# Kernel tuning notes

Hardware: AMD Instinct MI355X
Metric: run time of the kernel (lower is better)

The kernel has to match this reference:

```python
import jax, jax.numpy as jnp
import numpy as np

D_MODEL = 2048
N_HEADS = 8
HEAD_DIM = D_MODEL // N_HEADS
SCALING = HEAD_DIM ** -0.5


def setup_inputs() -> dict:
    key = jax.random.key(0)
    ks = jax.random.split(key, 9)
    B, S, D = 2, 2048, D_MODEL
    std = D ** -0.5
    inp = {"x": jax.random.normal(ks[0], (B, S, D), dtype=jnp.float32)}
    names = ["Wq", "Wk", "Wv", "Wo"]
    for i, n in enumerate(names):
        inp[n] = jax.random.normal(ks[1 + i], (D, D), dtype=jnp.float32) * std
        inp["b" + n[1]] = jax.random.normal(ks[5 + i], (D,), dtype=jnp.float32) * 0.01
    return inp


def reference(x, Wq, bq, Wk, bk, Wv, bv, Wo, bo):
    B, S, D = x.shape
    H, hd = N_HEADS, HEAD_DIM

    def proj(W, b):
        # nn.Linear: x @ W.T + b, then split heads -> [B, H, S, hd]
        y = jnp.einsum("bsd,ed->bse", x, W) + b
        return y.reshape(B, S, H, hd).transpose(0, 2, 1, 3)

    q = proj(Wq, bq)
    k = proj(Wk, bk)
    v = proj(Wv, bv)

    # scaled QK^T: [B, H, S, S]
    attn_weights = jnp.einsum("bhqd,bhkd->bhqk", q, k) * SCALING
    causal = jnp.tril(jnp.ones((S, S), dtype=bool))  # [S, S]
    attn_weights = jnp.where(causal[None, None], attn_weights, -jnp.inf)
    attn_probs = jax.nn.softmax(attn_weights, axis=-1)

    out = jnp.einsum("bhqk,bhkd->bhqd", attn_probs, v)  # [B, H, S, hd]
    out = out.transpose(0, 2, 1, 3).reshape(B, S, D)
    out = jnp.einsum("bsd,ed->bse", out, Wo) + bo
    return (out, attn_probs)
```

## Files before the change

### kernel.cpp

```cpp
#include <hip/hip_runtime.h>
#include <cstdint>
#include <cstddef>

typedef _Float16 f16;
typedef __attribute__((ext_vector_type(4))) _Float16 f16x4;
typedef __attribute__((ext_vector_type(8))) _Float16 f16x8;
typedef __attribute__((ext_vector_type(4))) float f32x4;

#define NB 2
#define SEQ 2048
#define DM 2048
#define NH 8
#define HD 256
#define MT (NB * SEQ)

#define QSCALE 0.09016844f
#define CEXP   23.08312065f

__device__ __forceinline__ void gload16(const f16* g, f16* l) {
    __builtin_amdgcn_global_load_lds(
        (const __attribute__((address_space(1))) uint32_t*)(const void*)g,
        (__attribute__((address_space(3))) uint32_t*)(void*)l,
        16, 0, 0);
}

__global__ __launch_bounds__(256) void k_cvt5(
    const float* __restrict__ x, const float* __restrict__ Wq,
    const float* __restrict__ Wk, const float* __restrict__ Wv,
    const float* __restrict__ Wo,
    f16* __restrict__ xh, f16* __restrict__ Wqh, f16* __restrict__ Wkh,
    f16* __restrict__ Wvh, f16* __restrict__ Woh) {
    const int total = (MT * DM + 4 * DM * DM) / 4;
    for (int q = blockIdx.x * blockDim.x + threadIdx.x; q < total;
         q += gridDim.x * blockDim.x) {
        int i = q * 4;
        const float* src; f16* dst; int off;
        if (i < MT * DM) { src = x; dst = xh; off = i; }
        else {
            int j = i - MT * DM;
            int w = j >> 22;
            off = j & ((1 << 22) - 1);
            src = (w == 0) ? Wq : (w == 1) ? Wk : (w == 2) ? Wv : Wo;
            dst = (w == 0) ? Wqh : (w == 1) ? Wkh : (w == 2) ? Wvh : Woh;
        }
        f32x4 v = *(const f32x4*)(src + off);
        f16x4 h;
        h[0] = (f16)v[0]; h[1] = (f16)v[1]; h[2] = (f16)v[2]; h[3] = (f16)v[3];
        *(f16x4*)(dst + off) = h;
    }
}

__device__ __forceinline__ void stage3(const f16* __restrict__ A,
                                       const f16* __restrict__ B,
                                       int m0, int n0, int k0,
                                       f16* AL, f16* BL, int tid, int half) {
#pragma unroll
    for (int jj = 0; jj < 2; ++jj) {
        int j = half * 2 + jj;
        int flat = j * 4096 + tid * 8;
        int r = flat >> 6, c = flat & 63;
        int cs = c ^ ((r & 7) << 3);
        gload16(A + (size_t)(m0 + r) * DM + k0 + cs,
                AL + j * 4096 + (tid >> 6) * 512);
    }
    {
        int j = half;
        int flat = j * 4096 + tid * 8;
        int r = flat >> 6, c = flat & 63;
        int cs = c ^ ((r & 7) << 3);
        gload16(B + (size_t)(n0 + r) * DM + k0 + cs,
                BL + j * 4096 + (tid >> 6) * 512);
    }
}

__device__ __forceinline__ f16x8 rdfrag(const f16* buf, int rowbase, int lr,
                                        int lg, int kk) {
    int row = rowbase + lr;
    int c = (kk * 32 + lg * 8) ^ ((lr & 7) << 3);
    return *(const f16x8*)&buf[row * 64 + c];
}

__device__ __forceinline__ void gemm256x128_core(const f16* __restrict__ A,
                                                 const f16* __restrict__ B,
                                                 int m0, int n0,
                                                 f16* AL, f16* BL,
                                                 f32x4 acc[4][4]) {
    const int tid = threadIdx.x, wave = tid >> 6, lane = tid & 63;
    const int wm = wave >> 1, wn = wave & 1;
    const int lr = lane & 15, lg = lane >> 4;
    const int nt = DM / 64;

    stage3(A, B, m0, n0, 0, AL, BL, tid, 0);
    stage3(A, B, m0, n0, 0, AL, BL, tid, 1);
    stage3(A, B, m0, n0, 64, AL + 16384, BL + 8192, tid, 0);
    stage3(A, B, m0, n0, 64, AL + 16384, BL + 8192, tid, 1);
    asm volatile("s_waitcnt vmcnt(6)" ::: "memory");
    __builtin_amdgcn_s_barrier();
    __builtin_amdgcn_sched_barrier(0);

    for (int kt = 0; kt < nt; ++kt) {
        const f16* Ab = AL + (kt % 3) * 16384;
        const f16* Bb = BL + (kt % 3) * 8192;
        const int arb = wm * 64, brb = wn * 64;

#pragma unroll
        for (int ph = 0; ph < 2; ++ph) {
            f16x8 af[4], bf[4];
#pragma unroll
            for (int mf = 0; mf < 4; ++mf)
                af[mf] = rdfrag(Ab, arb + mf * 16, lr, lg, ph);
#pragma unroll
            for (int nf = 0; nf < 4; ++nf)
                bf[nf] = rdfrag(Bb, brb + nf * 16, lr, lg, ph);

            if (kt + 2 < nt)
                stage3(A, B, m0, n0, (kt + 2) * 64,
                       AL + ((kt + 2) % 3) * 16384,
                       BL + ((kt + 2) % 3) * 8192, tid, ph);

            __builtin_amdgcn_sched_barrier(0);
            if (ph == 1) {
                if (kt + 2 < nt)
                    asm volatile("s_waitcnt vmcnt(6)" ::: "memory");
                else if (kt + 1 < nt)
                    asm volatile("s_waitcnt vmcnt(0)" ::: "memory");
            }
            __builtin_amdgcn_s_barrier();
            asm volatile("s_waitcnt lgkmcnt(0)" ::: "memory");
            __builtin_amdgcn_sched_barrier(0);

            __builtin_amdgcn_s_setprio(1);
#pragma unroll
            for (int mi = 0; mi < 4; ++mi)
#pragma unroll
                for (int nj = 0; nj < 4; ++nj)
                    acc[mi][nj] = __builtin_amdgcn_mfma_f32_16x16x32_f16(
                        af[mi], bf[nj], acc[mi][nj], 0, 0, 0);
            __builtin_amdgcn_s_setprio(0);
            __builtin_amdgcn_s_barrier();
        }
    }
}

__global__ __launch_bounds__(512, 1) void k_proj_qkv(
    const f16* __restrict__ xh, const f16* __restrict__ Wq,
    const f16* __restrict__ Wk, const f16* __restrict__ Wv,
    const float* __restrict__ bq, const float* __restrict__ bk,
    const float* __restrict__ bv,
    f16* __restrict__ Qh, f16* __restrict__ Kh, f16* __restrict__ Vth) {
    __shared__ __align__(16) f16 AL[3 * 16384];
    __shared__ __align__(16) f16 BL[3 * 8192];
    const int mode = blockIdx.z;
    const f16* W = (mode == 0) ? Wq : (mode == 1) ? Wk : Wv;
    const float* bias = (mode == 0) ? bq : (mode == 1) ? bk : bv;

    const int phys = blockIdx.x + 16 * blockIdx.y;
    const int xcdq = phys & 7, idx = phys >> 3;
    const int m0 = (xcdq * 2 + (idx >> 4)) * 256;
    const int n0 = (idx & 15) * 128;

    f32x4 acc[4][4];
#pragma unroll
    for (int mi = 0; mi < 4; ++mi)
#pragma unroll
        for (int nj = 0; nj < 4; ++nj) acc[mi][nj] = (f32x4){0.f, 0.f, 0.f, 0.f};

    gemm256x128_core(xh, W, m0, n0, AL, BL, acc);

    const int lane = threadIdx.x & 63, wave = threadIdx.x >> 6;
    const int wm = wave >> 1, wn = wave & 1;
    const int lr = lane & 15, lg = lane >> 4;
#pragma unroll
    for (int nj = 0; nj < 4; ++nj) {
        int n = n0 + wn * 64 + nj * 16 + lr;
        float bb = bias[n];
        int h = n >> 8, d = n & 255;
#pragma unroll
        for (int mi = 0; mi < 4; ++mi) {
#pragma unroll
            for (int i = 0; i < 4; ++i) {
                int m = m0 + wm * 64 + mi * 16 + lg * 4 + i;
                int b = m >> 11, s = m & 2047;
                float v = acc[mi][nj][i] + bb;
                size_t bh = (size_t)(b * NH + h);
                if (mode == 0)
                    Qh[((bh * SEQ + s) << 8) + d] = (f16)(v * QSCALE);
                else if (mode == 1)
                    Kh[((bh * SEQ + s) << 8) + d] = (f16)v;
                else
                    Vth[((bh * HD + d) << 11) + s] = (f16)v;
            }
        }
    }
}

__global__ __launch_bounds__(512, 1) void k_proj_o(
    const f16* __restrict__ Oh, const f16* __restrict__ Wo,
    const float* __restrict__ bo, float* __restrict__ out) {
    __shared__ __align__(16) f16 AL[3 * 16384];
    __shared__ __align__(16) f16 BL[3 * 8192];

    const int phys = blockIdx.x + 16 * blockIdx.y;
    const int xcdq = phys & 7, idx = phys >> 3;
    const int m0 = (xcdq * 2 + (idx >> 4)) * 256;
    const int n0 = (idx & 15) * 128;

    f32x4 acc[4][4];
#pragma unroll
    for (int mi = 0; mi < 4; ++mi)
#pragma unroll
        for (int nj = 0; nj < 4; ++nj) acc[mi][nj] = (f32x4){0.f, 0.f, 0.f, 0.f};

    gemm256x128_core(Oh, Wo, m0, n0, AL, BL, acc);

    const int lane = threadIdx.x & 63, wave = threadIdx.x >> 6;
    const int wm = wave >> 1, wn = wave & 1;
    const int lr = lane & 15, lg = lane >> 4;
#pragma unroll
    for (int nj = 0; nj < 4; ++nj) {
        int n = n0 + wn * 64 + nj * 16 + lr;
        float bb = bo[n];
#pragma unroll
        for (int mi = 0; mi < 4; ++mi) {
#pragma unroll
            for (int i = 0; i < 4; ++i) {
                int m = m0 + wm * 64 + mi * 16 + lg * 4 + i;
                out[(size_t)m * DM + n] = acc[mi][nj][i] + bb;
            }
        }
    }
}

__device__ __forceinline__ void stageK(const f16* __restrict__ Kb, int kt,
                                       f16* buf, int wave, int lane) {
#pragma unroll
    for (int j = 0; j < 8; ++j) {
        int base = (j * 4 + wave) << 9;
        int flat = base + (lane << 3);
        int r = flat >> 8;
        int c = (flat & 255) ^ ((r & 7) << 3);
        gload16(Kb + (size_t)(kt * 64 + r) * HD + c, buf + base);
    }
}
__device__ __forceinline__ void stageV(const f16* __restrict__ Vb, int kt,
                                       f16* buf, int wave, int lane) {
#pragma unroll
    for (int j = 0; j < 8; ++j) {
        int base = (j * 4 + wave) << 9;
        int flat = base + (lane << 3);
        int rv = flat >> 6;
        int cv = (flat & 63) ^ ((rv & 3) << 3);
        gload16(Vb + ((size_t)rv << 11) + kt * 64 + cv, buf + base);
    }
}

__global__ __launch_bounds__(256, 2) void k_attn(
    const f16* __restrict__ Qh, const f16* __restrict__ Kh,
    const f16* __restrict__ Vth, float* __restrict__ P,
    f16* __restrict__ Oh) {
    __shared__ __align__(16) f16 B0[64 * 256];
    __shared__ __align__(16) f16 B1[64 * 256];
    __shared__ __align__(16) f16 Ps[4][16][72];

    const int bid = blockIdx.x;
    const int xcd = bid & 7;
    const int slot = bid >> 3;
    const int psel = slot >> 5;
    const int s5 = slot & 31;
    const int qb = psel ? s5 : (31 - s5);
    const int bhid = xcd * 2 + psel;
    const int b = bhid >> 3, h = bhid & 7;

    const int q0 = qb * 64;
    const int tid = threadIdx.x, wave = tid >> 6, lane = tid & 63;
    const int lr = lane & 15, lg = lane >> 4;
    const size_t bh = (size_t)bhid;
    const f16* Qb = Qh + (bh << 19);
    const f16* Kb = Kh + (bh << 19);
    const f16* Vb = Vth + (bh << 19);
    float* Pb = P + (bh << 22);

    const int kswz = (lr & 7) << 3;
    const int vswz = (lr & 3) << 3;

    f16x8 aq[8];
    {
        const f16* qrow = Qb + (size_t)(q0 + wave * 16 + lr) * HD + lg * 8;
#pragma unroll
        for (int kk = 0; kk < 8; ++kk) aq[kk] = *(const f16x8*)(qrow + kk * 32);
    }

    const int rowb = q0 + wave * 16 + lg * 4;
    const int nt = qb + 1;

    float psum[4] = {0.f, 0.f, 0.f, 0.f};

    stageK(Kb, 0, B0, wave, lane);
    for (int kt = 0; kt < nt; ++kt) {
        f16* cur = (kt & 1) ? B1 : B0;
        f16* nxt = (kt & 1) ? B0 : B1;
        if (kt + 1 < nt) {
            stageK(Kb, kt + 1, nxt, wave, lane);
            asm volatile("s_waitcnt vmcnt(8)" ::: "memory");
        } else {
            asm volatile("s_waitcnt vmcnt(0)" ::: "memory");
        }
        __builtin_amdgcn_s_barrier();
        __builtin_amdgcn_sched_barrier(0);

        f32x4 s[4];
#pragma unroll
        for (int nj = 0; nj < 4; ++nj) s[nj] = (f32x4){0.f, 0.f, 0.f, 0.f};
        __builtin_amdgcn_s_setprio(1);
#pragma unroll
        for (int kk = 0; kk < 8; ++kk) {
#pragma unroll
            for (int nj = 0; nj < 4; ++nj) {
                f16x8 bk = *(const f16x8*)&cur[(nj * 16 + lr) * 256 +
                                               ((kk * 32 + lg * 8) ^ kswz)];
                s[nj] = __builtin_amdgcn_mfma_f32_16x16x32_f16(aq[kk], bk, s[nj], 0, 0, 0);
            }
        }
        __builtin_amdgcn_s_setprio(0);
        if (kt < qb) {
#pragma unroll
            for (int i = 0; i < 4; ++i)
#pragma unroll
                for (int nj = 0; nj < 4; ++nj)
                    psum[i] += exp2f(s[nj][i] - CEXP);
        } else {
            const int colb = kt * 64 + lr;
#pragma unroll
            for (int i = 0; i < 4; ++i) {
                int row = rowb + i;
#pragma unroll
                for (int nj = 0; nj < 4; ++nj)
                    psum[i] += (colb + nj * 16 <= row) ? exp2f(s[nj][i] - CEXP) : 0.f;
            }
        }
        asm volatile("" ::: "memory");
        __builtin_amdgcn_s_barrier();
        __builtin_amdgcn_sched_barrier(0);
    }

    float inv[4];
#pragma unroll
    for (int i = 0; i < 4; ++i) {
        float l = psum[i];
        l += __shfl_xor(l, 1);
        l += __shfl_xor(l, 2);
        l += __shfl_xor(l, 4);
        l += __shfl_xor(l, 8);
        inv[i] = 1.f / l;
    }

    f32x4 o[16];
#pragma unroll
    for (int n = 0; n < 16; ++n) o[n] = (f32x4){0.f, 0.f, 0.f, 0.f};

    stageK(Kb, 0, B0, wave, lane);
    for (int kt = 0; kt < nt; ++kt) {
        stageV(Vb, kt, B1, wave, lane);
        if (kt == 0) asm volatile("s_waitcnt vmcnt(8)" ::: "memory");
        else         asm volatile("s_waitcnt vmcnt(10)" ::: "memory");
        __builtin_amdgcn_s_barrier();
        __builtin_amdgcn_sched_barrier(0);

        f32x4 s[4];
#pragma unroll
        for (int nj = 0; nj < 4; ++nj) s[nj] = (f32x4){0.f, 0.f, 0.f, 0.f};
        __builtin_amdgcn_s_setprio(1);
#pragma unroll
        for (int kk = 0; kk < 8; ++kk) {
#pragma unroll
            for (int nj = 0; nj < 4; ++nj) {
                f16x8 bk = *(const f16x8*)&B0[(nj * 16 + lr) * 256 +
                                              ((kk * 32 + lg * 8) ^ kswz)];
                s[nj] = __builtin_amdgcn_mfma_f32_16x16x32_f16(aq[kk], bk, s[nj], 0, 0, 0);
            }
        }
        __builtin_amdgcn_s_setprio(0);
        if (kt < qb) {
#pragma unroll
            for (int i = 0; i < 4; ++i)
#pragma unroll
                for (int nj = 0; nj < 4; ++nj) {
                    float pv = exp2f(s[nj][i] - CEXP) * inv[i];
                    Ps[wave][lg * 4 + i][nj * 16 + lr] = (f16)pv;
                }
        } else {
#pragma unroll
            for (int i = 0; i < 4; ++i) {
                int row = rowb + i;
#pragma unroll
                for (int nj = 0; nj < 4; ++nj) {
                    int col = kt * 64 + nj * 16 + lr;
                    float pv = (col <= row) ? exp2f(s[nj][i] - CEXP) * inv[i] : 0.f;
                    Ps[wave][lg * 4 + i][nj * 16 + lr] = (f16)pv;
                }
            }
        }
        asm volatile("s_waitcnt vmcnt(0)" ::: "memory");
        __builtin_amdgcn_s_barrier();
        __builtin_amdgcn_sched_barrier(0);

        if (kt + 1 < nt) stageK(Kb, kt + 1, B0, wave, lane);

        __builtin_amdgcn_s_setprio(1);
#pragma unroll
        for (int kk2 = 0; kk2 < 2; ++kk2) {
            f16x8 pa = *(const f16x8*)&Ps[wave][lr][kk2 * 32 + lg * 8];
#pragma unroll
            for (int n = 0; n < 16; ++n) {
                f16x8 bv = *(const f16x8*)&B1[(n * 16 + lr) * 64 +
                                              ((kk2 * 32 + lg * 8) ^ vswz)];
                o[n] = __builtin_amdgcn_mfma_f32_16x16x32_f16(pa, bv, o[n], 0, 0, 0);
            }
        }
        __builtin_amdgcn_s_setprio(0);

#pragma unroll
        for (int h2 = 0; h2 < 2; ++h2) {
            int rr = h2 * 8 + (lane >> 3);
            int cc = (lane & 7) * 8;
            f16x8 ph = *(const f16x8*)&Ps[wave][rr][cc];
            int row = q0 + wave * 16 + rr;
            float* dst = Pb + (size_t)row * SEQ + kt * 64 + cc;
            f32x4 lo = {(float)ph[0], (float)ph[1], (float)ph[2], (float)ph[3]};
            f32x4 hi = {(float)ph[4], (float)ph[5], (float)ph[6], (float)ph[7]};
            *(f32x4*)dst = lo;
            *(f32x4*)(dst + 4) = hi;
        }

        asm volatile("" ::: "memory");
        __builtin_amdgcn_s_barrier();
        __builtin_amdgcn_sched_barrier(0);
    }

    int kstart = (qb + 1) * 64;
    if (kstart < SEQ) {
        f32x4 z = (f32x4){0.f, 0.f, 0.f, 0.f};
        for (int r = 0; r < 64; ++r) {
            float* rp = Pb + (size_t)(q0 + r) * SEQ;
            for (int c = kstart + tid * 4; c < SEQ; c += 1024)
                *(f32x4*)(rp + c) = z;
        }
    }

#pragma unroll
    for (int n = 0; n < 16; ++n) {
#pragma unroll
        for (int i = 0; i < 4; ++i) {
            int row = rowb + i;
            int d = n * 16 + lr;
            Oh[((size_t)b * SEQ + row) * DM + h * HD + d] = (f16)o[n][i];
        }
    }
}

extern "C" void kernel_launch(void* const* d_in, const int* in_sizes, int n_in,
                              void* d_out, int out_size, void* d_ws, size_t ws_size,
                              hipStream_t stream) {
    const float* x  = (const float*)d_in[0];
    const float* Wq = (const float*)d_in[1];
    const float* bq = (const float*)d_in[2];
    const float* Wk = (const float*)d_in[3];
    const float* bk = (const float*)d_in[4];
    const float* Wv = (const float*)d_in[5];
    const float* bv = (const float*)d_in[6];
    const float* Wo = (const float*)d_in[7];
    const float* bo = (const float*)d_in[8];

    float* out  = (float*)d_out;
    float* Pout = out + (size_t)MT * DM;

    f16* xh  = (f16*)Pout;
    f16* Wqh = xh + (size_t)MT * DM;
    f16* Wkh = Wqh + (size_t)DM * DM;
    f16* Wvh = Wkh + (size_t)DM * DM;

    f16* ws16 = (f16*)d_ws;
    f16* Woh = ws16;
    f16* Qh  = Woh + (size_t)DM * DM;
    f16* Kh  = Qh + (size_t)8388608;
    f16* Vth = Kh + (size_t)8388608;
    f16* Oh  = Vth + (size_t)8388608;
    if (ws_size < (size_t)(4194304 + 4 * 8388608) * sizeof(f16)) return;

    k_cvt5<<<2048, 256, 0, stream>>>(x, Wq, Wk, Wv, Wo, xh, Wqh, Wkh, Wvh, Woh);

    dim3 g1(DM / 128, MT / 256, 3);
    k_proj_qkv<<<g1, 512, 0, stream>>>(xh, Wqh, Wkh, Wvh, bq, bk, bv, Qh, Kh, Vth);

    k_attn<<<dim3(512), 256, 0, stream>>>(Qh, Kh, Vth, Pout, Oh);

    dim3 g3(DM / 128, MT / 256, 1);
    k_proj_o<<<g3, 512, 0, stream>>>(Oh, Woh, bo, out);
}
```

Baseline: 349.4 us.

## Split softmax row-sum pass into separate kernel parallelized over key chunks

The first pass of the attention kernel, which computes softmax denominators with a fixed-max exp, moves into a new k_rowsum kernel. That kernel splits each query block's key tiles across 4 chunks in a second grid dimension and writes per-chunk partial sums to workspace. The attention kernel then reads and adds the four partials instead of recomputing QK^T for the denominator. This raises parallelism for the causal-imbalanced first pass, but it adds a kernel launch, drops the double-buffered K staging in that pass, and reloads Q and K in a separate kernel.

```diff
diff --git a/kernel.cpp b/kernel.cpp
--- a/kernel.cpp
+++ b/kernel.cpp
@@ -254,10 +254,97 @@
     }
 }
 
+__global__ __launch_bounds__(256, 4) void k_rowsum(
+    const f16* __restrict__ Qh, const f16* __restrict__ Kh,
+    float* __restrict__ partial) {
+    __shared__ __align__(16) f16 Kl[64 * 256];
+
+    const int bid = blockIdx.x;
+    const int xcd = bid & 7;
+    const int slot = bid >> 3;
+    const int psel = slot >> 5;
+    const int s5 = slot & 31;
+    const int qb = psel ? s5 : (31 - s5);
+    const int bhid = xcd * 2 + psel;
+    const int chunk = blockIdx.y;
+
+    const int q0 = qb * 64;
+    const int tid = threadIdx.x, wave = tid >> 6, lane = tid & 63;
+    const int lr = lane & 15, lg = lane >> 4;
+    const size_t bh = (size_t)bhid;
+    const f16* Qb = Qh + (bh << 19);
+    const f16* Kb = Kh + (bh << 19);
+
+    const int kswz = (lr & 7) << 3;
+
+    f16x8 aq[8];
+    {
+        const f16* qrow = Qb + (size_t)(q0 + wave * 16 + lr) * HD + lg * 8;
+#pragma unroll
+        for (int kk = 0; kk < 8; ++kk) aq[kk] = *(const f16x8*)(qrow + kk * 32);
+    }
+    const int rowb = q0 + wave * 16 + lg * 4;
+    const int nt = qb + 1;
+
+    float psum[4] = {0.f, 0.f, 0.f, 0.f};
+
+    for (int t = chunk; t < nt; t += 4) {
+        stageK(Kb, t, Kl, wave, lane);
+        asm volatile("s_waitcnt vmcnt(0)" ::: "memory");
+        __builtin_amdgcn_s_barrier();
+        __builtin_amdgcn_sched_barrier(0);
+
+        f32x4 s[4];
+#pragma unroll
+        for (int nj = 0; nj < 4; ++nj) s[nj] = (f32x4){0.f, 0.f, 0.f, 0.f};
+        __builtin_amdgcn_s_setprio(1);
+#pragma unroll
+        for (int kk = 0; kk < 8; ++kk) {
+#pragma unroll
+            for (int nj = 0; nj < 4; ++nj) {
+                f16x8 bk = *(const f16x8*)&Kl[(nj * 16 + lr) * 256 +
+                                              ((kk * 32 + lg * 8) ^ kswz)];
+                s[nj] = __builtin_amdgcn_mfma_f32_16x16x32_f16(aq[kk], bk, s[nj], 0, 0, 0);
+            }
+        }
+        __builtin_amdgcn_s_setprio(0);
+        if (t < qb) {
+#pragma unroll
+            for (int i = 0; i < 4; ++i)
+#pragma unroll
+                for (int nj = 0; nj < 4; ++nj)
+                    psum[i] += exp2f(s[nj][i] - CEXP);
+        } else {
+            const int colb = t * 64 + lr;
+#pragma unroll
+            for (int i = 0; i < 4; ++i) {
+                int row = rowb + i;
+#pragma unroll
+                for (int nj = 0; nj < 4; ++nj)
+                    psum[i] += (colb + nj * 16 <= row) ? exp2f(s[nj][i] - CEXP) : 0.f;
+            }
+        }
+        asm volatile("" ::: "memory");
+        __builtin_amdgcn_s_barrier();
+        __builtin_amdgcn_sched_barrier(0);
+    }
+
+#pragma unroll
+    for (int i = 0; i < 4; ++i) {
+        float l = psum[i];
+        l += __shfl_xor(l, 1);
+        l += __shfl_xor(l, 2);
+        l += __shfl_xor(l, 4);
+        l += __shfl_xor(l, 8);
+        if (lr == 0)
+            partial[((bh * SEQ) + rowb + i) * 4 + chunk] = l;
+    }
+}
+
 __global__ __launch_bounds__(256, 2) void k_attn(
     const f16* __restrict__ Qh, const f16* __restrict__ Kh,
-    const f16* __restrict__ Vth, float* __restrict__ P,
-    f16* __restrict__ Oh) {
+    const f16* __restrict__ Vth, const float* __restrict__ partial,
+    float* __restrict__ P, f16* __restrict__ Oh) {
     __shared__ __align__(16) f16 B0[64 * 256];
     __shared__ __align__(16) f16 B1[64 * 256];
     __shared__ __align__(16) f16 Ps[4][16][72];
@@ -293,65 +380,11 @@
     const int rowb = q0 + wave * 16 + lg * 4;
     const int nt = qb + 1;
 
-    float psum[4] = {0.f, 0.f, 0.f, 0.f};
-
-    stageK(Kb, 0, B0, wave, lane);
-    for (int kt = 0; kt < nt; ++kt) {
-        f16* cur = (kt & 1) ? B1 : B0;
-        f16* nxt = (kt & 1) ? B0 : B1;
-        if (kt + 1 < nt) {
-            stageK(Kb, kt + 1, nxt, wave, lane);
-            asm volatile("s_waitcnt vmcnt(8)" ::: "memory");
-        } else {
-            asm volatile("s_waitcnt vmcnt(0)" ::: "memory");
-        }
-        __builtin_amdgcn_s_barrier();
-        __builtin_amdgcn_sched_barrier(0);
-
-        f32x4 s[4];
-#pragma unroll
-        for (int nj = 0; nj < 4; ++nj) s[nj] = (f32x4){0.f, 0.f, 0.f, 0.f};
-        __builtin_amdgcn_s_setprio(1);
-#pragma unroll
-        for (int kk = 0; kk < 8; ++kk) {
-#pragma unroll
-            for (int nj = 0; nj < 4; ++nj) {
-                f16x8 bk = *(const f16x8*)&cur[(nj * 16 + lr) * 256 +
-                                               ((kk * 32 + lg * 8) ^ kswz)];
-                s[nj] = __builtin_amdgcn_mfma_f32_16x16x32_f16(aq[kk], bk, s[nj], 0, 0, 0);
-            }
-        }
-        __builtin_amdgcn_s_setprio(0);
-        if (kt < qb) {
-#pragma unroll
-            for (int i = 0; i < 4; ++i)
-#pragma unroll
-                for (int nj = 0; nj < 4; ++nj)
-                    psum[i] += exp2f(s[nj][i] - CEXP);
-        } else {
-            const int colb = kt * 64 + lr;
-#pragma unroll
-            for (int i = 0; i < 4; ++i) {
-                int row = rowb + i;
-#pragma unroll
-                for (int nj = 0; nj < 4; ++nj)
-                    psum[i] += (colb + nj * 16 <= row) ? exp2f(s[nj][i] - CEXP) : 0.f;
-            }
-        }
-        asm volatile("" ::: "memory");
-        __builtin_amdgcn_s_barrier();
-        __builtin_amdgcn_sched_barrier(0);
-    }
-
     float inv[4];
 #pragma unroll
     for (int i = 0; i < 4; ++i) {
-        float l = psum[i];
-        l += __shfl_xor(l, 1);
-        l += __shfl_xor(l, 2);
-        l += __shfl_xor(l, 4);
-        l += __shfl_xor(l, 8);
-        inv[i] = 1.f / l;
+        f32x4 p = *(const f32x4*)&partial[((bh * SEQ) + rowb + i) * 4];
+        inv[i] = 1.f / (p[0] + p[1] + p[2] + p[3]);
     }
 
     f32x4 o[16];
@@ -485,14 +518,17 @@
     f16* Kh  = Qh + (size_t)8388608;
     f16* Vth = Kh + (size_t)8388608;
     f16* Oh  = Vth + (size_t)8388608;
-    if (ws_size < (size_t)(4194304 + 4 * 8388608) * sizeof(f16)) return;
+    float* partial = (float*)(Oh + (size_t)8388608);
+    if (ws_size < (size_t)(4194304 + 4 * 8388608) * sizeof(f16) + 524288) return;
 
     k_cvt5<<<2048, 256, 0, stream>>>(x, Wq, Wk, Wv, Wo, xh, Wqh, Wkh, Wvh, Woh);
 
     dim3 g1(DM / 128, MT / 256, 3);
     k_proj_qkv<<<g1, 512, 0, stream>>>(xh, Wqh, Wkh, Wvh, bq, bk, bv, Qh, Kh, Vth);
 
-    k_attn<<<dim3(512), 256, 0, stream>>>(Qh, Kh, Vth, Pout, Oh);
+    k_rowsum<<<dim3(512, 4), 256, 0, stream>>>(Qh, Kh, partial);
+
+    k_attn<<<dim3(512), 256, 0, stream>>>(Qh, Kh, Vth, partial, Pout, Oh);
 
     dim3 g3(DM / 128, MT / 256, 1);
     k_proj_o<<<g3, 512, 0, stream>>>(Oh, Woh, bo, out);
```

Result: slower. 363.7 us (+4.1%).
